# Kernel tuning notes

Hardware: AMD Instinct MI355X
Metric: run time of the kernel (lower is better)

Reference implementation:

```python
import jax, jax.numpy as jnp
import numpy as np

B, S, DIM = 1, 2048, 4096
NH, NKV, HD = 32, 8, 128
REPEATS = NH // NKV
ROPE_THETA = 10000.0


def setup_inputs() -> dict:
    key = jax.random.key(0)
    ks = jax.random.split(key, 6)
    x = jax.random.normal(ks[0], (B, S, DIM), jnp.float32) * 0.02
    wq = jax.random.normal(ks[1], (NH * HD, DIM), jnp.float32) * 0.02
    wk = jax.random.normal(ks[2], (NKV * HD, DIM), jnp.float32) * 0.02
    wv = jax.random.normal(ks[3], (NKV * HD, DIM), jnp.float32) * 0.02
    wo = jax.random.normal(ks[4], (DIM, NH * HD), jnp.float32) * 0.02
    # rotary frequencies (real cos/sin form of complex freqs_cis)
    inv_freq = 1.0 / (ROPE_THETA ** (jnp.arange(0, HD, 2, dtype=jnp.float32) / HD))
    ang = jnp.arange(S, dtype=jnp.float32)[:, None] * inv_freq[None, :]  # [S, HD//2]
    freqs_cos = jnp.cos(ang)
    freqs_sin = jnp.sin(ang)
    positions = jnp.arange(S, dtype=jnp.int32)  # prompt phase: all positions
    # additive causal mask
    mask = jnp.where(jnp.tril(jnp.ones((S, S), bool)), 0.0, -1e9).astype(jnp.float32)
    cache_k = jnp.zeros((B, S, NKV, HD), jnp.float32)
    cache_v = jnp.zeros((B, S, NKV, HD), jnp.float32)
    return dict(x=x, wq=wq, wk=wk, wv=wv, wo=wo, freqs_cos=freqs_cos,
                freqs_sin=freqs_sin, cache_k=cache_k, cache_v=cache_v,
                positions=positions, mask=mask)


def apply_rope(t, cos, sin):
    # t: [b, s, h, d]; pairs are (d0,d1),(d2,d3),... matching view_as_complex
    tr = t[..., 0::2]
    ti = t[..., 1::2]
    c = cos[None, :, None, :]
    s = sin[None, :, None, :]
    out_r = tr * c - ti * s
    out_i = tr * s + ti * c
    return jnp.stack([out_r, out_i], axis=-1).reshape(t.shape)


def reference(x, wq, wk, wv, wo, freqs_cos, freqs_sin, cache_k, cache_v, positions, mask):
    b, s, _ = x.shape
    xq = jnp.einsum('bsd,od->bso', x, wq).reshape(b, s, NH, HD)
    xk = jnp.einsum('bsd,od->bso', x, wk).reshape(b, s, NKV, HD)
    xv = jnp.einsum('bsd,od->bso', x, wv).reshape(b, s, NKV, HD)
    xq = apply_rope(xq, freqs_cos, freqs_sin)
    xk = apply_rope(xk, freqs_cos, freqs_sin)
    # KV-cache scatter (prompt phase writes; output uses fresh xk/xv here)
    cache_k = cache_k.at[:, positions].set(xk)
    cache_v = cache_v.at[:, positions].set(xv)
    # GQA: repeat_interleave kv heads to match query heads
    k = jnp.repeat(xk, REPEATS, axis=2).transpose(0, 2, 1, 3)  # [b, NH, s, HD]
    v = jnp.repeat(xv, REPEATS, axis=2).transpose(0, 2, 1, 3)
    q = xq.transpose(0, 2, 1, 3)
    scale = HD ** -0.5
    scores = jnp.einsum('bhqd,bhkd->bhqk', q, k) * scale + mask[None, None]
    probs = jax.nn.softmax(scores.astype(jnp.float32), axis=-1).astype(q.dtype)
    out = jnp.einsum('bhqk,bhkd->bhqd', probs, v)
    out = out.transpose(0, 2, 1, 3).reshape(b, s, NH * HD)
    return jnp.einsum('bso,do->bsd', out, wo)
```

## Files before the change

### kernel.cpp

```cpp
#include <hip/hip_runtime.h>
#include <hip/hip_bf16.h>
#include <stdint.h>

typedef __bf16 bf16_t;
typedef __attribute__((ext_vector_type(8))) __bf16 bf16x8;
typedef __attribute__((ext_vector_type(4))) float f32x4;
typedef __attribute__((ext_vector_type(8))) unsigned short u16x8;

#define S_LEN 2048
#define DIM   4096
#define QKVN  6144
#define NHEAD 32
#define HDIM  128

typedef __attribute__((address_space(1))) unsigned int as1_u32;
typedef __attribute__((address_space(3))) unsigned int as3_u32;

__device__ __forceinline__ unsigned short f2bf(float f) {
  unsigned u = __builtin_bit_cast(unsigned, f);
  u += 0x7fffu + ((u >> 16) & 1u);
  return (unsigned short)(u >> 16);
}

__device__ __forceinline__ void gload_lds16(const void* g, void* l) {
  __builtin_amdgcn_global_load_lds(
      (as1_u32*)(unsigned long long)(uintptr_t)g,
      (as3_u32*)(unsigned int)(uintptr_t)l,
      16, 0, 0);
}

__global__ __launch_bounds__(256) void cvt5_kernel(const float* __restrict__ x,
                                                   const float* __restrict__ wq,
                                                   const float* __restrict__ wk,
                                                   const float* __restrict__ wv,
                                                   const float* __restrict__ wo,
                                                   ushort4* __restrict__ xb,
                                                   ushort4* __restrict__ wqkvb,
                                                   ushort4* __restrict__ wob) {
  const long N0 = 2097152;
  const long N1 = N0 + 4194304;
  const long N2 = N1 + 1048576;
  const long N3 = N2 + 1048576;
  const long N4 = N3 + 4194304;
  long idx = (long)blockIdx.x * 256 + threadIdx.x;
  long stride = (long)gridDim.x * 256;
  for (long i = idx; i < N4; i += stride) {
    const float4* s; ushort4* d; long o;
    if (i < N0)      { s = (const float4*)x;  d = xb;              o = i; }
    else if (i < N1) { s = (const float4*)wq; d = wqkvb;           o = i - N0; }
    else if (i < N2) { s = (const float4*)wk; d = wqkvb + 4194304; o = i - N1; }
    else if (i < N3) { s = (const float4*)wv; d = wqkvb + 5242880; o = i - N2; }
    else             { s = (const float4*)wo; d = wob;             o = i - N3; }
    float4 v = s[o];
    ushort4 r;
    r.x = f2bf(v.x); r.y = f2bf(v.y); r.z = f2bf(v.z); r.w = f2bf(v.w);
    d[o] = r;
  }
}

__device__ __forceinline__ bf16x8 fld(const char* half, int row, int chunk) {
  return *(const bf16x8*)(half + row * 128 + ((chunk ^ (row & 7)) << 4));
}

template <int OUTF32>
__global__ __launch_bounds__(512, 2) void gemm8q(const bf16_t* __restrict__ A,
                                                 const bf16_t* __restrict__ B,
                                                 void* __restrict__ Cout,
                                                 int M, int N, int K, int nxt) {
  __shared__ char lds[147456];
  const int tid = threadIdx.x;
  const int lane = tid & 63, w = tid >> 6;
  const int wm = w >> 2, wn = w & 3;
  const int lg = lane >> 4, lr = lane & 15;
  const int nwg = gridDim.x;
  const int orig = blockIdx.x;
  const int wgid = (orig & 7) * (nwg >> 3) + (orig >> 3);
  const int bx = wgid % nxt, by = wgid / nxt;
  const long rowA = (long)by * 256;
  const long rowB = (long)bx * 192;

  f32x4 acc[8][3];
  const f32x4 z4 = {0.f, 0.f, 0.f, 0.f};
#pragma unroll
  for (int i = 0; i < 8; ++i)
#pragma unroll
    for (int j = 0; j < 3; ++j) acc[i][j] = z4;

  const int r0 = tid >> 3, sl = tid & 7;
  const long xo  = (long)((sl ^ (r0 & 7)) << 3);
  const long aof = (rowA + r0) * (long)K + xo;
  const long bof = (rowB + r0) * (long)K + xo;
  const long j1  = (long)64 * K;
  const long h1  = (long)128 * K;
  const int ld0 = tid * 16, ld1 = (tid + 512) * 16, ld2 = (tid + 1024) * 16;

#define QSTG_A(K0, HALF, BUF3)                                                 \
  { char* hp = lds + (BUF3) * 32768 + (HALF) * 16384;                          \
    gload_lds16(A + aof + (HALF) * h1 + (K0),      hp + ld0);                  \
    gload_lds16(A + aof + (HALF) * h1 + j1 + (K0), hp + ld1); }
#define QSTG_B(K0, DBUF)                                                       \
  { char* bp = lds + 98304 + (DBUF) * 24576;                                   \
    gload_lds16(B + bof + (K0),          bp + ld0);                            \
    gload_lds16(B + bof + j1 + (K0),     bp + ld1);                            \
    gload_lds16(B + bof + 2 * j1 + (K0), bp + ld2); }

  const int nt = K >> 6;
  const int brow = wn * 48;

  QSTG_A(0, 0, 0); QSTG_A(0, 1, 0); QSTG_B(0, 0);
  QSTG_A(64, 0, 1); QSTG_A(64, 1, 1); QSTG_B(64, 1);
  asm volatile("s_waitcnt vmcnt(7)" ::: "memory");
  __builtin_amdgcn_s_barrier();

  bf16x8 af[8][2], bf_[3][2];

  for (int t = 0; t < nt; ++t) {
    const int a3 = t % 3, s3 = (t + 2) % 3, d = t & 1;
    const char* Ah = lds + a3 * 32768 + wm * 16384;
    const char* Br = lds + 98304 + d * 24576;
    const int k2 = (t + 2) << 6;
#pragma unroll
    for (int m = 0; m < 2; ++m) {
      af[m][0] = fld(Ah, m * 16 + lr, lg);
      af[m][1] = fld(Ah, m * 16 + lr, 4 + lg);
    }
#pragma unroll
    for (int n = 0; n < 3; ++n) {
      bf_[n][0] = fld(Br, brow + n * 16 + lr, lg);
      bf_[n][1] = fld(Br, brow + n * 16 + lr, 4 + lg);
    }
    if (t + 2 < nt) QSTG_A(k2, 0, s3);
    __builtin_amdgcn_s_barrier();
    asm volatile("s_waitcnt lgkmcnt(0)" ::: "memory");
    __builtin_amdgcn_sched_barrier(0);
    __builtin_amdgcn_s_setprio(1);
#pragma unroll
    for (int m = 0; m < 2; ++m)
#pragma unroll
      for (int n = 0; n < 3; ++n) {
        acc[m][n] = __builtin_amdgcn_mfma_f32_16x16x32_bf16(af[m][0], bf_[n][0], acc[m][n], 0, 0, 0);
        acc[m][n] = __builtin_amdgcn_mfma_f32_16x16x32_bf16(af[m][1], bf_[n][1], acc[m][n], 0, 0, 0);
      }
    __builtin_amdgcn_s_setprio(0);
    __builtin_amdgcn_s_barrier();
#pragma unroll
    for (int m = 2; m < 4; ++m) {
      af[m][0] = fld(Ah, m * 16 + lr, lg);
      af[m][1] = fld(Ah, m * 16 + lr, 4 + lg);
    }
    if (t + 2 < nt) QSTG_A(k2, 1, s3);
    __builtin_amdgcn_s_barrier();
    asm volatile("s_waitcnt lgkmcnt(0)" ::: "memory");
    __builtin_amdgcn_sched_barrier(0);
    __builtin_amdgcn_s_setprio(1);
#pragma unroll
    for (int m = 2; m < 4; ++m)
#pragma unroll
      for (int n = 0; n < 3; ++n) {
        acc[m][n] = __builtin_amdgcn_mfma_f32_16x16x32_bf16(af[m][0], bf_[n][0], acc[m][n], 0, 0, 0);
        acc[m][n] = __builtin_amdgcn_mfma_f32_16x16x32_bf16(af[m][1], bf_[n][1], acc[m][n], 0, 0, 0);
      }
    __builtin_amdgcn_s_setprio(0);
    __builtin_amdgcn_s_barrier();
#pragma unroll
    for (int m = 4; m < 6; ++m) {
      af[m][0] = fld(Ah, m * 16 + lr, lg);
      af[m][1] = fld(Ah, m * 16 + lr, 4 + lg);
    }
    if (t + 2 < nt) QSTG_B(k2, d);
    __builtin_amdgcn_s_barrier();
    asm volatile("s_waitcnt lgkmcnt(0)" ::: "memory");
    __builtin_amdgcn_sched_barrier(0);
    __builtin_amdgcn_s_setprio(1);
#pragma unroll
    for (int m = 4; m < 6; ++m)
#pragma unroll
      for (int n = 0; n < 3; ++n) {
        acc[m][n] = __builtin_amdgcn_mfma_f32_16x16x32_bf16(af[m][0], bf_[n][0], acc[m][n], 0, 0, 0);
        acc[m][n] = __builtin_amdgcn_mfma_f32_16x16x32_bf16(af[m][1], bf_[n][1], acc[m][n], 0, 0, 0);
      }
    __builtin_amdgcn_s_setprio(0);
    __builtin_amdgcn_s_barrier();
#pragma unroll
    for (int m = 6; m < 8; ++m) {
      af[m][0] = fld(Ah, m * 16 + lr, lg);
      af[m][1] = fld(Ah, m * 16 + lr, 4 + lg);
    }
    __builtin_amdgcn_s_barrier();
    asm volatile("s_waitcnt lgkmcnt(0)" ::: "memory");
    __builtin_amdgcn_sched_barrier(0);
    __builtin_amdgcn_s_setprio(1);
#pragma unroll
    for (int m = 6; m < 8; ++m)
#pragma unroll
      for (int n = 0; n < 3; ++n) {
        acc[m][n] = __builtin_amdgcn_mfma_f32_16x16x32_bf16(af[m][0], bf_[n][0], acc[m][n], 0, 0, 0);
        acc[m][n] = __builtin_amdgcn_mfma_f32_16x16x32_bf16(af[m][1], bf_[n][1], acc[m][n], 0, 0, 0);
      }
    __builtin_amdgcn_s_setprio(0);
    if (t + 2 < nt) {
      asm volatile("s_waitcnt vmcnt(7)" ::: "memory");
    } else {
      asm volatile("s_waitcnt vmcnt(0)" ::: "memory");
    }
    __builtin_amdgcn_s_barrier();
  }
#undef QSTG_A
#undef QSTG_B

  const long crow = rowA + wm * 128;
  const long ccol = rowB + wn * 48;
  unsigned short* C = (unsigned short*)Cout;
#pragma unroll
  for (int mf = 0; mf < 8; ++mf)
#pragma unroll
    for (int j = 0; j < 4; ++j) {
      long row = crow + mf * 16 + lg * 4 + j;
      unsigned short* cp = C + row * N + ccol + lr;
#pragma unroll
      for (int nf = 0; nf < 3; ++nf) cp[nf * 16] = f2bf(acc[mf][nf][j]);
    }
}

template <int OUTF32>
__global__ __launch_bounds__(512, 2) void gemm2p(const bf16_t* __restrict__ A,
                                                 const bf16_t* __restrict__ B,
                                                 void* __restrict__ Cout,
                                                 int M, int N, int K, int nxt) {
  __shared__ char lds[147456];
  const int tid = threadIdx.x;
  const int lane = tid & 63, w = tid >> 6;
  const int wm = w >> 1, wn = w & 1;
  const int lg = lane >> 4, lr = lane & 15;
  const int nwg = gridDim.x;
  const int orig = blockIdx.x;
  const int wgid = (orig & 7) * (nwg >> 3) + (orig >> 3);
  const int bx = wgid % nxt, by = wgid / nxt;
  const long rowA = (long)by * 256;
  const long rowB = (long)bx * 128;

  f32x4 acc[4][4];
  const f32x4 z4 = {0.f, 0.f, 0.f, 0.f};
#pragma unroll
  for (int i = 0; i < 4; ++i)
#pragma unroll
    for (int j = 0; j < 4; ++j) acc[i][j] = z4;

  const int r0 = tid >> 3, sl = tid & 7;
  const long xo  = (long)((sl ^ (r0 & 7)) << 3);
  const long aof = (rowA + r0) * (long)K + xo;
  const long bof = (rowB + r0) * (long)K + xo;
  const long r64 = (long)64 * K;

#define PSTG_A(K0, BUF)                                                        \
  { char* ap = lds + (BUF) * 32768;                                            \
    gload_lds16(A + aof + (K0),           ap + tid * 16);                      \
    gload_lds16(A + aof + r64 + (K0),     ap + (tid + 512) * 16);              \
    gload_lds16(A + aof + 2 * r64 + (K0), ap + (tid + 1024) * 16);             \
    gload_lds16(A + aof + 3 * r64 + (K0), ap + (tid + 1536) * 16); }
#define PSTG_B(K0, BUF)                                                        \
  { char* bp = lds + 98304 + (BUF) * 16384;                                    \
    gload_lds16(B + bof + (K0),       bp + tid * 16);                          \
    gload_lds16(B + bof + r64 + (K0), bp + (tid + 512) * 16); }

  const int nt = K >> 6;

  PSTG_A(0, 0); PSTG_B(0, 0); PSTG_A(64, 1); PSTG_B(64, 1);
  asm volatile("s_waitcnt vmcnt(6)" ::: "memory");
  __builtin_amdgcn_s_barrier();

  bf16x8 af[4][2], bf_[4][2];

  for (int t = 0; t < nt; ++t) {
    const int b3 = t % 3, s3 = (t + 2) % 3;
    const char* Ab = lds + b3 * 32768;
    const char* Bb = lds + 98304 + b3 * 16384;
    const int arow = wm * 64, brow = wn * 64;
    const int k2 = (t + 2) << 6;
#pragma unroll
    for (int m = 0; m < 4; ++m) {
      af[m][0] = fld(Ab, arow + m * 16 + lr, lg);
      af[m][1] = fld(Ab, arow + m * 16 + lr, 4 + lg);
    }
#pragma unroll
    for (int n = 0; n < 2; ++n) {
      bf_[n][0] = fld(Bb, brow + n * 16 + lr, lg);
      bf_[n][1] = fld(Bb, brow + n * 16 + lr, 4 + lg);
    }
    if (t + 2 < nt) PSTG_A(k2, s3);
    __builtin_amdgcn_s_barrier();
    asm volatile("s_waitcnt lgkmcnt(0)" ::: "memory");
    __builtin_amdgcn_sched_barrier(0);
    __builtin_amdgcn_s_setprio(1);
#pragma unroll
    for (int m = 0; m < 4; ++m)
#pragma unroll
      for (int n = 0; n < 2; ++n) {
        acc[m][n] = __builtin_amdgcn_mfma_f32_16x16x32_bf16(af[m][0], bf_[n][0], acc[m][n], 0, 0, 0);
        acc[m][n] = __builtin_amdgcn_mfma_f32_16x16x32_bf16(af[m][1], bf_[n][1], acc[m][n], 0, 0, 0);
      }
    __builtin_amdgcn_s_setprio(0);
    __builtin_amdgcn_s_barrier();
#pragma unroll
    for (int n = 2; n < 4; ++n) {
      bf_[n][0] = fld(Bb, brow + n * 16 + lr, lg);
      bf_[n][1] = fld(Bb, brow + n * 16 + lr, 4 + lg);
    }
    if (t + 2 < nt) PSTG_B(k2, s3);
    __builtin_amdgcn_s_barrier();
    asm volatile("s_waitcnt lgkmcnt(0)" ::: "memory");
    __builtin_amdgcn_sched_barrier(0);
    __builtin_amdgcn_s_setprio(1);
#pragma unroll
    for (int m = 0; m < 4; ++m)
#pragma unroll
      for (int n = 2; n < 4; ++n) {
        acc[m][n] = __builtin_amdgcn_mfma_f32_16x16x32_bf16(af[m][0], bf_[n][0], acc[m][n], 0, 0, 0);
        acc[m][n] = __builtin_amdgcn_mfma_f32_16x16x32_bf16(af[m][1], bf_[n][1], acc[m][n], 0, 0, 0);
      }
    __builtin_amdgcn_s_setprio(0);
    if (t + 2 < nt) {
      asm volatile("s_waitcnt vmcnt(6)" ::: "memory");
    } else {
      asm volatile("s_waitcnt vmcnt(0)" ::: "memory");
    }
    __builtin_amdgcn_s_barrier();
  }
#undef PSTG_A
#undef PSTG_B

  const long crow = rowA + wm * 64;
  const long ccol = rowB + wn * 64;
  if (OUTF32) {
    float* C = (float*)Cout;
#pragma unroll
    for (int mf = 0; mf < 4; ++mf)
#pragma unroll
      for (int j = 0; j < 4; ++j) {
        long row = crow + mf * 16 + lg * 4 + j;
        float* cp = C + row * N + ccol + lr;
#pragma unroll
        for (int nf = 0; nf < 4; ++nf) cp[nf * 16] = acc[mf][nf][j];
      }
  } else {
    unsigned short* C = (unsigned short*)Cout;
#pragma unroll
    for (int mf = 0; mf < 4; ++mf)
#pragma unroll
      for (int j = 0; j < 4; ++j) {
        long row = crow + mf * 16 + lg * 4 + j;
        unsigned short* cp = C + row * N + ccol + lr;
#pragma unroll
        for (int nf = 0; nf < 4; ++nf) cp[nf * 16] = f2bf(acc[mf][nf][j]);
      }
  }
}

__global__ __launch_bounds__(256) void rope_kernel(unsigned int* __restrict__ qkv32,
                                                   const float* __restrict__ cosb,
                                                   const float* __restrict__ sinb) {
  int t = blockIdx.x * 256 + threadIdx.x;
  int i  = t & 63;
  int sh = t >> 6;
  int hh = sh % 40;
  int s  = sh / 40;
  int col2 = (hh < 32) ? (hh * 64 + i) : (2048 + (hh - 32) * 64 + i);
  unsigned int* p = qkv32 + (long)s * (QKVN / 2) + col2;
  unsigned int v = *p;
  float tr = __builtin_bit_cast(float, (v & 0xffffu) << 16);
  float ti = __builtin_bit_cast(float, v & 0xffff0000u);
  float c  = cosb[s * 64 + i];
  float sn = sinb[s * 64 + i];
  float orr = tr * c - ti * sn;
  float oi  = tr * sn + ti * c;
  *p = (unsigned int)f2bf(orr) | ((unsigned int)f2bf(oi) << 16);
}

__global__ __launch_bounds__(256) void vtrans_kernel(const bf16_t* __restrict__ qkv,
                                                     bf16_t* __restrict__ vT) {
  const int kh = blockIdx.x;
  const int hd = threadIdx.x & 127;
  const int s0 = blockIdx.y * 16 + (threadIdx.x >> 7) * 8;
  u16x8 v;
#pragma unroll
  for (int e = 0; e < 8; ++e)
    v[e] = *(const unsigned short*)(qkv + (long)(s0 + e) * QKVN + 5120 + kh * HDIM + hd);
  *(u16x8*)(vT + ((long)kh * HDIM + hd) * S_LEN + s0) = v;
}

__global__ __launch_bounds__(512) void attn_kernel(const bf16_t* __restrict__ qkv,
                                                   const bf16_t* __restrict__ vT,
                                                   unsigned short* __restrict__ ob) {
  __shared__ bf16_t Kt[2][64 * 128];
  __shared__ bf16_t Vt[2][128 * 64];
  __shared__ bf16_t Pl[8 * 16 * 64];
  const int h  = blockIdx.x;
  const int qi = 15 - (int)blockIdx.y;
  const int qb = qi * 128;
  const int kh = h >> 2;
  const int tid = threadIdx.x, lane = tid & 63, w = tid >> 6;
  const int lg = lane >> 4, lr = lane & 15;
  const int qrow0 = qb + w * 16;

  bf16x8 qf[4];
  const bf16_t* qptr = qkv + (long)(qrow0 + lr) * QKVN + h * HDIM + lg * 8;
#pragma unroll
  for (int kk = 0; kk < 4; ++kk) qf[kk] = *(const bf16x8*)(qptr + kk * 32);

  const f32x4 z4 = {0.f, 0.f, 0.f, 0.f};
  f32x4 oacc[8];
#pragma unroll
  for (int c = 0; c < 8; ++c) oacc[c] = z4;
  float m[4]    = {-1e30f, -1e30f, -1e30f, -1e30f};
  float lsum[4] = {0.f, 0.f, 0.f, 0.f};

  char* PlB = (char*)Pl + w * 2048;
  const float SCL2 = 0.08838834764831845f * 1.44269504088896f;
  const int ntiles = 2 * qi + 2;
  const int wqmax = qrow0 + 15;

#define STAGE_KV(T, BUF)                                                       \
  {                                                                            \
    const int kvs = (T) * 64;                                                  \
    _Pragma("unroll")                                                          \
    for (int it = 0; it < 2; ++it) {                                           \
      int cch = tid + it * 512;                                                \
      int r = cch >> 4, c = cch & 15;                                          \
      gload_lds16(qkv + (long)(kvs + r) * QKVN + 4096 + kh * HDIM              \
                      + ((c ^ (r & 7)) * 8),                                   \
                  (char*)Kt[BUF] + cch * 16);                                  \
    }                                                                          \
    _Pragma("unroll")                                                          \
    for (int it = 0; it < 2; ++it) {                                           \
      int cch = tid + it * 512;                                                \
      int hd2 = cch >> 3, c = cch & 7;                                         \
      gload_lds16(vT + ((long)kh * HDIM + hd2) * S_LEN + kvs                   \
                      + ((c ^ (hd2 & 7)) * 8),                                 \
                  (char*)Vt[BUF] + cch * 16);                                  \
    }                                                                          \
  }

  STAGE_KV(0, 0);
  STAGE_KV(1, 1);
  asm volatile("s_waitcnt vmcnt(4)" ::: "memory");
  __builtin_amdgcn_s_barrier();

  for (int t = 0; t < ntiles; ++t) {
    const int kv0 = t * 64;
    const int d = t & 1;
    if (kv0 <= wqmax) {
      char* KtB = (char*)Kt[d];
      char* VtB = (char*)Vt[d];

      f32x4 sf[4];
#pragma unroll
      for (int f = 0; f < 4; ++f) {
        f32x4 a = z4;
        int n = f * 16 + lr;
        int rb = n * 256, sw = (n & 7) << 4;
#pragma unroll
        for (int kk = 0; kk < 4; ++kk) {
          bf16x8 kf = *(const bf16x8*)(KtB + rb + (((kk * 4 + lg) * 16) ^ sw));
          a = __builtin_amdgcn_mfma_f32_16x16x32_bf16(qf[kk], kf, a, 0, 0, 0);
        }
        sf[f] = a;
      }

      float sv[4][4], mx[4];
      if (kv0 + 63 <= qrow0) {
#pragma unroll
        for (int j = 0; j < 4; ++j) {
#pragma unroll
          for (int f = 0; f < 4; ++f) sv[j][f] = sf[f][j] * SCL2;
          float t0 = fmaxf(fmaxf(sv[j][0], sv[j][1]), fmaxf(sv[j][2], sv[j][3]));
          t0 = fmaxf(t0, __shfl_xor(t0, 1));
          t0 = fmaxf(t0, __shfl_xor(t0, 2));
          t0 = fmaxf(t0, __shfl_xor(t0, 4));
          t0 = fmaxf(t0, __shfl_xor(t0, 8));
          mx[j] = t0;
        }
      } else {
#pragma unroll
        for (int j = 0; j < 4; ++j) {
          int qrow = qrow0 + lg * 4 + j;
#pragma unroll
          for (int f = 0; f < 4; ++f) {
            float s = sf[f][j] * SCL2;
            if (kv0 + f * 16 + lr > qrow) s = -1e9f;
            sv[j][f] = s;
          }
          float t0 = fmaxf(fmaxf(sv[j][0], sv[j][1]), fmaxf(sv[j][2], sv[j][3]));
          t0 = fmaxf(t0, __shfl_xor(t0, 1));
          t0 = fmaxf(t0, __shfl_xor(t0, 2));
          t0 = fmaxf(t0, __shfl_xor(t0, 4));
          t0 = fmaxf(t0, __shfl_xor(t0, 8));
          mx[j] = t0;
        }
      }
      float g = fmaxf(fmaxf(mx[0] - m[0], mx[1] - m[1]),
                      fmaxf(mx[2] - m[2], mx[3] - m[3]));
      if (__any(g > 0.f)) {
#pragma unroll
        for (int j = 0; j < 4; ++j) {
          float mn = fmaxf(m[j], mx[j]);
          float sc;
          asm("v_exp_f32 %0, %1" : "=v"(sc) : "v"(m[j] - mn));
          lsum[j] *= sc;
          m[j] = mn;
#pragma unroll
          for (int c = 0; c < 8; ++c) oacc[c][j] *= sc;
        }
      }
#pragma unroll
      for (int j = 0; j < 4; ++j) {
        float p[4];
#pragma unroll
        for (int f = 0; f < 4; ++f)
          asm("v_exp_f32 %0, %1" : "=v"(p[f]) : "v"(sv[j][f] - m[j]));
        float ps = (p[0] + p[1]) + (p[2] + p[3]);
        ps += __shfl_xor(ps, 1);
        ps += __shfl_xor(ps, 2);
        ps += __shfl_xor(ps, 4);
        ps += __shfl_xor(ps, 8);
        lsum[j] += ps;
        int row = lg * 4 + j;
        int swp = (row & 7) << 4;
#pragma unroll
        for (int f = 0; f < 4; ++f)
          *(unsigned short*)(PlB + row * 128 + (((f * 16 + lr) * 2) ^ swp)) = f2bf(p[f]);
      }

      bf16x8 pfr[2];
#pragma unroll
      for (int kk = 0; kk < 2; ++kk)
        pfr[kk] = *(const bf16x8*)(PlB + lr * 128 + (((kk * 4 + lg) * 16) ^ ((lr & 7) << 4)));
#pragma unroll
      for (int c = 0; c < 8; ++c) {
        int hd = c * 16 + lr;
        int rb = hd * 128, sw = (hd & 7) << 4;
#pragma unroll
        for (int kk = 0; kk < 2; ++kk) {
          bf16x8 vf = *(const bf16x8*)(VtB + rb + (((kk * 4 + lg) * 16) ^ sw));
          oacc[c] = __builtin_amdgcn_mfma_f32_16x16x32_bf16(pfr[kk], vf, oacc[c], 0, 0, 0);
        }
      }
    }
    __builtin_amdgcn_s_barrier();
    if (t + 2 < ntiles) {
      STAGE_KV(t + 2, d);
      asm volatile("s_waitcnt vmcnt(4)" ::: "memory");
    } else {
      asm volatile("s_waitcnt vmcnt(0)" ::: "memory");
    }
    __builtin_amdgcn_s_barrier();
  }
#undef STAGE_KV

  float rl[4];
#pragma unroll
  for (int j = 0; j < 4; ++j) rl[j] = 1.f / lsum[j];
#pragma unroll
  for (int c = 0; c < 8; ++c)
#pragma unroll
    for (int j = 0; j < 4; ++j) {
      long row = qrow0 + lg * 4 + j;
      ob[row * 4096 + h * 128 + c * 16 + lr] = f2bf(oacc[c][j] * rl[j]);
    }
}

extern "C" void kernel_launch(void* const* d_in, const int* in_sizes, int n_in,
                              void* d_out, int out_size, void* d_ws, size_t ws_size,
                              hipStream_t stream) {
  const float* x  = (const float*)d_in[0];
  const float* wq = (const float*)d_in[1];
  const float* wk = (const float*)d_in[2];
  const float* wv = (const float*)d_in[3];
  const float* wo = (const float*)d_in[4];
  const float* fc = (const float*)d_in[5];
  const float* fs = (const float*)d_in[6];

  char* ws = (char*)d_ws;
  bf16_t* xb    = (bf16_t*)(ws + 0);
  bf16_t* wqkvb = (bf16_t*)(ws + 16777216);
  bf16_t* wob   = (bf16_t*)(ws + 67108864);
  bf16_t* qkv   = (bf16_t*)(ws + 100663296);
  bf16_t* ob    = (bf16_t*)(ws + 125829120);
  bf16_t* vT    = (bf16_t*)(ws + 0);

  cvt5_kernel<<<2048, 256, 0, stream>>>(x, wq, wk, wv, wo,
                                        (ushort4*)xb, (ushort4*)wqkvb, (ushort4*)wob);

  gemm8q<0><<<256, 512, 0, stream>>>(xb, wqkvb, qkv, 2048, 6144, 4096, 32);
  vtrans_kernel<<<dim3(8, 128), 256, 0, stream>>>(qkv, vT);
  rope_kernel<<<20480, 256, 0, stream>>>((unsigned int*)qkv, fc, fs);
  attn_kernel<<<dim3(32, 16), 512, 0, stream>>>(qkv, vT, (unsigned short*)ob);
  gemm2p<1><<<256, 512, 0, stream>>>(ob, wob, d_out, 2048, 4096, 4096, 32);
}
```

Measured before the change: 320.1 us.

## Merge V-transpose and RoPE launches; defer softmax row reductions in attention

Combines the V-transpose and RoPE kernels into one launch, split by block index. The two touch disjoint columns of the QKV buffer, so this saves a launch and its tail. In the attention loop, each lane now keeps its own partial row sum and max. The cross-lane max shuffle runs only when some lane's local max exceeds the running max, and the sum shuffle runs once after the loop instead of every tile. This cuts per-tile shuffle and latency work in the softmax, and the partial sums stay consistent because every lane rescales against the shared reduced max.

```diff
diff --git a/kernel.cpp b/kernel.cpp
--- a/kernel.cpp
+++ b/kernel.cpp
@@ -356,36 +356,37 @@
   }
 }
 
-__global__ __launch_bounds__(256) void rope_kernel(unsigned int* __restrict__ qkv32,
+__global__ __launch_bounds__(256) void prep_kernel(bf16_t* __restrict__ qkv,
+                                                   bf16_t* __restrict__ vT,
                                                    const float* __restrict__ cosb,
                                                    const float* __restrict__ sinb) {
-  int t = blockIdx.x * 256 + threadIdx.x;
-  int i  = t & 63;
-  int sh = t >> 6;
-  int hh = sh % 40;
-  int s  = sh / 40;
-  int col2 = (hh < 32) ? (hh * 64 + i) : (2048 + (hh - 32) * 64 + i);
-  unsigned int* p = qkv32 + (long)s * (QKVN / 2) + col2;
-  unsigned int v = *p;
-  float tr = __builtin_bit_cast(float, (v & 0xffffu) << 16);
-  float ti = __builtin_bit_cast(float, v & 0xffff0000u);
-  float c  = cosb[s * 64 + i];
-  float sn = sinb[s * 64 + i];
-  float orr = tr * c - ti * sn;
-  float oi  = tr * sn + ti * c;
-  *p = (unsigned int)f2bf(orr) | ((unsigned int)f2bf(oi) << 16);
-}
-
-__global__ __launch_bounds__(256) void vtrans_kernel(const bf16_t* __restrict__ qkv,
-                                                     bf16_t* __restrict__ vT) {
-  const int kh = blockIdx.x;
-  const int hd = threadIdx.x & 127;
-  const int s0 = blockIdx.y * 16 + (threadIdx.x >> 7) * 8;
-  u16x8 v;
-#pragma unroll
-  for (int e = 0; e < 8; ++e)
-    v[e] = *(const unsigned short*)(qkv + (long)(s0 + e) * QKVN + 5120 + kh * HDIM + hd);
-  *(u16x8*)(vT + ((long)kh * HDIM + hd) * S_LEN + s0) = v;
+  const int bid = blockIdx.x;
+  if (bid < 1024) {
+    const int kh = bid & 7;
+    const int hd = threadIdx.x & 127;
+    const int s0 = (bid >> 3) * 16 + (threadIdx.x >> 7) * 8;
+    u16x8 v;
+#pragma unroll
+    for (int e = 0; e < 8; ++e)
+      v[e] = *(const unsigned short*)(qkv + (long)(s0 + e) * QKVN + 5120 + kh * HDIM + hd);
+    *(u16x8*)(vT + ((long)kh * HDIM + hd) * S_LEN + s0) = v;
+  } else {
+    int t = (bid - 1024) * 256 + threadIdx.x;
+    int i  = t & 63;
+    int sh = t >> 6;
+    int hh = sh % 40;
+    int s  = sh / 40;
+    int col2 = (hh < 32) ? (hh * 64 + i) : (2048 + (hh - 32) * 64 + i);
+    unsigned int* p = (unsigned int*)qkv + (long)s * (QKVN / 2) + col2;
+    unsigned int v = *p;
+    float tr = __builtin_bit_cast(float, (v & 0xffffu) << 16);
+    float ti = __builtin_bit_cast(float, v & 0xffff0000u);
+    float c  = cosb[s * 64 + i];
+    float sn = sinb[s * 64 + i];
+    float orr = tr * c - ti * sn;
+    float oi  = tr * sn + ti * c;
+    *p = (unsigned int)f2bf(orr) | ((unsigned int)f2bf(oi) << 16);
+  }
 }
 
 __global__ __launch_bounds__(512) void attn_kernel(const bf16_t* __restrict__ qkv,
@@ -411,8 +412,8 @@
   f32x4 oacc[8];
 #pragma unroll
   for (int c = 0; c < 8; ++c) oacc[c] = z4;
-  float m[4]    = {-1e30f, -1e30f, -1e30f, -1e30f};
-  float lsum[4] = {0.f, 0.f, 0.f, 0.f};
+  float m[4]     = {-1e30f, -1e30f, -1e30f, -1e30f};
+  float plsum[4] = {0.f, 0.f, 0.f, 0.f};
 
   char* PlB = (char*)Pl + w * 2048;
   const float SCL2 = 0.08838834764831845f * 1.44269504088896f;
@@ -466,18 +467,13 @@
         sf[f] = a;
       }
 
-      float sv[4][4], mx[4];
+      float sv[4][4], lmax[4];
       if (kv0 + 63 <= qrow0) {
 #pragma unroll
         for (int j = 0; j < 4; ++j) {
 #pragma unroll
           for (int f = 0; f < 4; ++f) sv[j][f] = sf[f][j] * SCL2;
-          float t0 = fmaxf(fmaxf(sv[j][0], sv[j][1]), fmaxf(sv[j][2], sv[j][3]));
-          t0 = fmaxf(t0, __shfl_xor(t0, 1));
-          t0 = fmaxf(t0, __shfl_xor(t0, 2));
-          t0 = fmaxf(t0, __shfl_xor(t0, 4));
-          t0 = fmaxf(t0, __shfl_xor(t0, 8));
-          mx[j] = t0;
+          lmax[j] = fmaxf(fmaxf(sv[j][0], sv[j][1]), fmaxf(sv[j][2], sv[j][3]));
         }
       } else {
 #pragma unroll
@@ -489,23 +485,23 @@
             if (kv0 + f * 16 + lr > qrow) s = -1e9f;
             sv[j][f] = s;
           }
-          float t0 = fmaxf(fmaxf(sv[j][0], sv[j][1]), fmaxf(sv[j][2], sv[j][3]));
+          lmax[j] = fmaxf(fmaxf(sv[j][0], sv[j][1]), fmaxf(sv[j][2], sv[j][3]));
+        }
+      }
+      float g = fmaxf(fmaxf(lmax[0] - m[0], lmax[1] - m[1]),
+                      fmaxf(lmax[2] - m[2], lmax[3] - m[3]));
+      if (__any(g > 0.f)) {
+#pragma unroll
+        for (int j = 0; j < 4; ++j) {
+          float t0 = lmax[j];
           t0 = fmaxf(t0, __shfl_xor(t0, 1));
           t0 = fmaxf(t0, __shfl_xor(t0, 2));
           t0 = fmaxf(t0, __shfl_xor(t0, 4));
           t0 = fmaxf(t0, __shfl_xor(t0, 8));
-          mx[j] = t0;
-        }
-      }
-      float g = fmaxf(fmaxf(mx[0] - m[0], mx[1] - m[1]),
-                      fmaxf(mx[2] - m[2], mx[3] - m[3]));
-      if (__any(g > 0.f)) {
-#pragma unroll
-        for (int j = 0; j < 4; ++j) {
-          float mn = fmaxf(m[j], mx[j]);
+          float mn = fmaxf(m[j], t0);
           float sc;
           asm("v_exp_f32 %0, %1" : "=v"(sc) : "v"(m[j] - mn));
-          lsum[j] *= sc;
+          plsum[j] *= sc;
           m[j] = mn;
 #pragma unroll
           for (int c = 0; c < 8; ++c) oacc[c][j] *= sc;
@@ -517,12 +513,7 @@
 #pragma unroll
         for (int f = 0; f < 4; ++f)
           asm("v_exp_f32 %0, %1" : "=v"(p[f]) : "v"(sv[j][f] - m[j]));
-        float ps = (p[0] + p[1]) + (p[2] + p[3]);
-        ps += __shfl_xor(ps, 1);
-        ps += __shfl_xor(ps, 2);
-        ps += __shfl_xor(ps, 4);
-        ps += __shfl_xor(ps, 8);
-        lsum[j] += ps;
+        plsum[j] += (p[0] + p[1]) + (p[2] + p[3]);
         int row = lg * 4 + j;
         int swp = (row & 7) << 4;
 #pragma unroll
@@ -558,7 +549,14 @@
 
   float rl[4];
 #pragma unroll
-  for (int j = 0; j < 4; ++j) rl[j] = 1.f / lsum[j];
+  for (int j = 0; j < 4; ++j) {
+    float s = plsum[j];
+    s += __shfl_xor(s, 1);
+    s += __shfl_xor(s, 2);
+    s += __shfl_xor(s, 4);
+    s += __shfl_xor(s, 8);
+    rl[j] = 1.f / s;
+  }
 #pragma unroll
   for (int c = 0; c < 8; ++c)
 #pragma unroll
@@ -591,8 +589,7 @@
                                         (ushort4*)xb, (ushort4*)wqkvb, (ushort4*)wob);
 
   gemm8q<0><<<256, 512, 0, stream>>>(xb, wqkvb, qkv, 2048, 6144, 4096, 32);
-  vtrans_kernel<<<dim3(8, 128), 256, 0, stream>>>(qkv, vT);
-  rope_kernel<<<20480, 256, 0, stream>>>((unsigned int*)qkv, fc, fs);
+  prep_kernel<<<21504, 256, 0, stream>>>(qkv, vT, fc, fs);
   attn_kernel<<<dim3(32, 16), 512, 0, stream>>>(qkv, vT, (unsigned short*)ob);
   gemm2p<1><<<256, 512, 0, stream>>>(ob, wob, d_out, 2048, 4096, 4096, 32);
 }
```

Measured after the change: 310.7 us. 1.03x faster.
